# Performance work log

Measured on AMD Instinct MI355X. Metric: run time of the kernel, lower is better.

The kernel has to match this reference:

```python
import jax, jax.numpy as jnp
import numpy as np
from jax import lax

B, L = 2, 1024
D_MODEL, D_STATE, EXPAND, D_CONV = 1024, 16, 2, 4
D_INNER = EXPAND * D_MODEL            # 2048
DT_RANK = (D_MODEL + 15) // 16        # 64


def setup_inputs() -> dict:
    key = jax.random.key(0)
    ks = jax.random.split(key, 8)
    g = lambda k, shape, s=0.02: jax.random.normal(k, shape, dtype=jnp.float32) * s
    # Mamba-style A init: A = -exp(A_log), A_log = log(1..d_state) per channel
    A_log = jnp.log(jnp.broadcast_to(
        jnp.arange(1, D_STATE + 1, dtype=jnp.float32), (D_INNER, D_STATE)))
    return {
        "x": jax.random.normal(ks[0], (B, L, D_MODEL), dtype=jnp.float32),
        "W_in": g(ks[1], (D_MODEL, 2 * D_INNER)),
        "conv_w": g(ks[2], (D_INNER, D_CONV), 0.1),
        "conv_b": jnp.zeros((D_INNER,), jnp.float32),
        "W_x": g(ks[3], (D_INNER, DT_RANK + 2 * D_STATE)),
        "W_dt": g(ks[4], (DT_RANK, D_INNER)),
        "b_dt": g(ks[5], (D_INNER,), 0.1),
        "A_log": A_log,
        "D_skip": jnp.ones((D_INNER,), jnp.float32),
        "W_out": g(ks[6], (D_INNER, D_MODEL)),
    }


def reference(x, W_in, conv_w, conv_b, W_x, W_dt, b_dt, A_log, D_skip, W_out):
    # in_proj -> (u, z): [B, L, D_INNER] each
    xz = x @ W_in
    u, z = xz[..., :D_INNER], xz[..., D_INNER:]

    # causal depthwise conv1d, kernel D_CONV (small fixed loop over taps)
    up = jnp.pad(u, ((0, 0), (D_CONV - 1, 0), (0, 0)))
    u = sum(up[:, k:k + L, :] * conv_w[:, k] for k in range(D_CONV)) + conv_b
    u = jax.nn.silu(u)

    # input-dependent dt, B, C
    x_dbl = u @ W_x                                    # [B, L, dt_rank + 2N]
    dt = x_dbl[..., :DT_RANK]
    Bm = x_dbl[..., DT_RANK:DT_RANK + D_STATE]         # [B, L, N]
    Cm = x_dbl[..., DT_RANK + D_STATE:]                # [B, L, N]
    delta = jax.nn.softplus(dt @ W_dt + b_dt)          # [B, L, D]

    A = -jnp.exp(A_log)                                # [D, N]
    deltaA = jnp.exp(jnp.einsum('bld,dn->bldn', delta, A))   # [B, L, D, N]
    dBu = (delta * u)[..., None] * Bm[:, :, None, :]          # [B, L, D, N]

    def step(h, inp):
        dA_t, dBu_t, c_t = inp                         # [B,D,N],[B,D,N],[B,N]
        h = dA_t * h + dBu_t
        y_t = jnp.einsum('bdn,bn->bd', h, c_t)
        return h, y_t

    h0 = jnp.zeros((B, D_INNER, D_STATE), x.dtype)
    _, ys = lax.scan(step, h0,
                     (deltaA.transpose(1, 0, 2, 3),
                      dBu.transpose(1, 0, 2, 3),
                      Cm.transpose(1, 0, 2)))
    y = ys.transpose(1, 0, 2) + u * D_skip             # [B, L, D_INNER]
    y = y * jax.nn.silu(z)                             # gated output
    return y @ W_out                                   # [B, L, D_MODEL]
```

## Files before the change

kernel.cpp:

```cpp
#include <hip/hip_runtime.h>


typedef unsigned short u16;
typedef unsigned int   u32;

#define B_SZ 2
#define L_SZ 1024
#define DM   1024
#define DI   2048
#define DS   16
#define DTR  64
#define NXD  96
#define NCHUNK 16
#define CL   64
#define KSPLIT 8
#define KC     256
#define OSPLIT 4

typedef __bf16 bf16x8 __attribute__((ext_vector_type(8)));
typedef float  f32x4  __attribute__((ext_vector_type(4)));

__device__ __forceinline__ u16 f2bf(float f) {
    u32 x = __float_as_uint(f);
    x += 0x7fffu + ((x >> 16) & 1u);
    return (u16)(x >> 16);
}
__device__ __forceinline__ float bf2f(u16 v) {
    return __uint_as_float(((u32)v) << 16);
}

__device__ __forceinline__ void gld_lds16(const u16* g, u16* l) {
    __builtin_amdgcn_global_load_lds(
        (const __attribute__((address_space(1))) u32*)g,
        (__attribute__((address_space(3))) u32*)l, 16, 0, 0);
}

__global__ __launch_bounds__(256) void gemm128u2(
    const u16* __restrict__ A, const u16* __restrict__ BT,
    float* __restrict__ Cf, u16* __restrict__ Cb,
    const float* __restrict__ bias,
    int M, int N, int K, int KCHUNK, int op)
{
    __shared__ u16 As0[128 * 32];
    __shared__ u16 Bs0[128 * 32];
    __shared__ u16 As1[128 * 32];
    __shared__ u16 Bs1[128 * 32];

    const int tid  = threadIdx.x;
    const int wave = tid >> 6;
    const int lane = tid & 63;
    const int q    = lane >> 4;
    const int r16  = lane & 15;
    const int wm   = (wave & 1) * 64;
    const int wn   = (wave >> 1) * 64;
    const int m0   = blockIdx.y * 128;
    const int n0   = blockIdx.x * 128;
    const int srow = tid >> 2;
    const int sseg = (tid & 3) * 8;
    const int kb   = blockIdx.z * KCHUNK;

    const u16* gA0 = A  + (size_t)(m0 + srow)      * K + sseg;
    const u16* gA1 = A  + (size_t)(m0 + 64 + srow) * K + sseg;
    const u16* gB0 = BT + (size_t)(n0 + srow)      * K + sseg;
    const u16* gB1 = BT + (size_t)(n0 + 64 + srow) * K + sseg;
    u16* lA0 = As0 + tid * 8;  u16* lA0b = As0 + 2048 + tid * 8;
    u16* lB0 = Bs0 + tid * 8;  u16* lB0b = Bs0 + 2048 + tid * 8;
    u16* lA1 = As1 + tid * 8;  u16* lA1b = As1 + 2048 + tid * 8;
    u16* lB1 = Bs1 + tid * 8;  u16* lB1b = Bs1 + 2048 + tid * 8;

    f32x4 acc[4][4];
#pragma unroll
    for (int s = 0; s < 4; ++s)
#pragma unroll
        for (int j = 0; j < 4; ++j) acc[s][j] = (f32x4){0.f, 0.f, 0.f, 0.f};

    for (int k0 = kb; k0 < kb + KCHUNK; k0 += 64) {
        __syncthreads();
        gld_lds16(gA0 + k0, lA0);
        gld_lds16(gA1 + k0, lA0b);
        gld_lds16(gB0 + k0, lB0);
        gld_lds16(gB1 + k0, lB0b);
        gld_lds16(gA0 + k0 + 32, lA1);
        gld_lds16(gA1 + k0 + 32, lA1b);
        gld_lds16(gB0 + k0 + 32, lB1);
        gld_lds16(gB1 + k0 + 32, lB1b);
        __syncthreads();

        bf16x8 af[4], bfr[4];
#pragma unroll
        for (int s = 0; s < 4; ++s)
            af[s] = *(const bf16x8*)(As0 + (wm + s * 16 + r16) * 32 + q * 8);
#pragma unroll
        for (int j = 0; j < 4; ++j)
            bfr[j] = *(const bf16x8*)(Bs0 + (wn + j * 16 + r16) * 32 + q * 8);
#pragma unroll
        for (int s = 0; s < 4; ++s)
#pragma unroll
            for (int j = 0; j < 4; ++j)
                acc[s][j] = __builtin_amdgcn_mfma_f32_16x16x32_bf16(
                    af[s], bfr[j], acc[s][j], 0, 0, 0);
#pragma unroll
        for (int s = 0; s < 4; ++s)
            af[s] = *(const bf16x8*)(As1 + (wm + s * 16 + r16) * 32 + q * 8);
#pragma unroll
        for (int j = 0; j < 4; ++j)
            bfr[j] = *(const bf16x8*)(Bs1 + (wn + j * 16 + r16) * 32 + q * 8);
#pragma unroll
        for (int s = 0; s < 4; ++s)
#pragma unroll
            for (int j = 0; j < 4; ++j)
                acc[s][j] = __builtin_amdgcn_mfma_f32_16x16x32_bf16(
                    af[s], bfr[j], acc[s][j], 0, 0, 0);
    }

#pragma unroll
    for (int s = 0; s < 4; ++s) {
        const int row0 = m0 + wm + s * 16 + q * 4;
#pragma unroll
        for (int j = 0; j < 4; ++j) {
            const int col = n0 + wn + j * 16 + r16;
            if (op == 0) {
                float* Cz = Cf + (size_t)blockIdx.z * M * N;
#pragma unroll
                for (int i = 0; i < 4; ++i)
                    Cz[(size_t)(row0 + i) * N + col] = acc[s][j][i];
            } else if (op == 1) {
                const float bv = bias[col];
#pragma unroll
                for (int i = 0; i < 4; ++i) {
                    float v = acc[s][j][i] + bv;
                    v = (v > 20.f) ? v : log1pf(__expf(v));
                    Cf[(size_t)(row0 + i) * N + col] = v;
                }
            } else {
#pragma unroll
                for (int i = 0; i < 4; ++i)
                    Cb[(size_t)(row0 + i) * N + col] = f2bf(acc[s][j][i]);
            }
        }
    }
}

__global__ __launch_bounds__(256) void reduce_out(
    const float* __restrict__ part, float* __restrict__ out, int n)
{
    const int i = (blockIdx.x * 256 + threadIdx.x) * 4;
    if (i >= n) return;
    f32x4 v = *(const f32x4*)(part + i);
#pragma unroll
    for (int s = 1; s < OSPLIT; ++s) {
        f32x4 p = *(const f32x4*)(part + (size_t)s * n + i);
        v.x += p.x; v.y += p.y; v.z += p.z; v.w += p.w;
    }
    *(f32x4*)(out + i) = v;
}

__global__ __launch_bounds__(256) void gemm_skinny_splitk(
    const u16* __restrict__ A, const u16* __restrict__ BT,
    float* __restrict__ Cpart, int M, int N, int K)
{
    constexpr int LDT = 40;
    __shared__ u16 As[128 * LDT];
    __shared__ u16 Bs[64 * LDT];

    const int tid  = threadIdx.x;
    const int wave = tid >> 6;
    const int lane = tid & 63;
    const int q    = lane >> 4;
    const int r16  = lane & 15;
    const int m0   = blockIdx.y * 128;
    const int n0   = blockIdx.x * 64;
    const int kcs  = blockIdx.z * KC;
    const int sr   = tid >> 2;
    const int ss   = (tid & 3) * 8;

    f32x4 acc[2][4];
#pragma unroll
    for (int s = 0; s < 2; ++s)
#pragma unroll
        for (int j = 0; j < 4; ++j) acc[s][j] = (f32x4){0.f, 0.f, 0.f, 0.f};

    const int  bcol   = n0 + sr;
    const bool bvalid = bcol < N;

    for (int k0 = kcs; k0 < kcs + KC; k0 += 32) {
        __syncthreads();
        uint4 a0 = *(const uint4*)(A + (size_t)(m0 + sr)      * K + k0 + ss);
        uint4 a1 = *(const uint4*)(A + (size_t)(m0 + 64 + sr) * K + k0 + ss);
        uint4 bv = make_uint4(0u, 0u, 0u, 0u);
        if (bvalid) bv = *(const uint4*)(BT + (size_t)bcol * K + k0 + ss);
        *(uint4*)(As + sr * LDT + ss)        = a0;
        *(uint4*)(As + (64 + sr) * LDT + ss) = a1;
        *(uint4*)(Bs + sr * LDT + ss)        = bv;
        __syncthreads();

        bf16x8 af[2], bfr[4];
#pragma unroll
        for (int s = 0; s < 2; ++s)
            af[s] = *(const bf16x8*)(As + (wave * 32 + s * 16 + r16) * LDT + q * 8);
#pragma unroll
        for (int j = 0; j < 4; ++j)
            bfr[j] = *(const bf16x8*)(Bs + (j * 16 + r16) * LDT + q * 8);
#pragma unroll
        for (int s = 0; s < 2; ++s)
#pragma unroll
            for (int j = 0; j < 4; ++j)
                acc[s][j] = __builtin_amdgcn_mfma_f32_16x16x32_bf16(
                    af[s], bfr[j], acc[s][j], 0, 0, 0);
    }

    float* Cp = Cpart + (size_t)blockIdx.z * M * N;
#pragma unroll
    for (int s = 0; s < 2; ++s) {
        const int row0 = m0 + wave * 32 + s * 16 + q * 4;
#pragma unroll
        for (int j = 0; j < 4; ++j) {
            const int col = n0 + j * 16 + r16;
            if (col < N) {
#pragma unroll
                for (int i = 0; i < 4; ++i)
                    Cp[(size_t)(row0 + i) * N + col] = acc[s][j][i];
            }
        }
    }
}

__global__ __launch_bounds__(256) void reduce_xdbl(
    const float* __restrict__ part, float* __restrict__ xdbl,
    u16* __restrict__ dtbf)
{
    const int i = blockIdx.x * 256 + threadIdx.x;
    const int row = i / NXD, col = i - row * NXD;
    float v = 0.f;
#pragma unroll
    for (int s = 0; s < KSPLIT; ++s)
        v += part[(size_t)s * (B_SZ * L_SZ * NXD) + i];
    xdbl[i] = v;
    if (col < DTR) dtbf[row * DTR + col] = f2bf(v);
}

__device__ __forceinline__ void tr_tile(
    const float* __restrict__ in, u16* __restrict__ out,
    int R, int C, int tr, int tc, int tid, float (*t)[33])
{
    const int tx = tid & 31, ty = tid >> 5;
    const int r0 = tr * 32, c0 = tc * 32;
#pragma unroll
    for (int i = 0; i < 4; ++i) {
        int r = r0 + ty + i * 8, c = c0 + tx;
        if (r < R && c < C) t[ty + i * 8][tx] = in[(size_t)r * C + c];
    }
    __syncthreads();
#pragma unroll
    for (int i = 0; i < 4; ++i) {
        int oR = c0 + ty + i * 8, oC = r0 + tx;
        if (oR < C && oC < R) out[(size_t)oR * R + oC] = f2bf(t[tx][ty + i * 8]);
    }
}

__global__ __launch_bounds__(256) void prep_kernel(
    const float* __restrict__ x,     u16* __restrict__ xbf,
    const float* __restrict__ W_in,  u16* __restrict__ winT,
    const float* __restrict__ W_out, u16* __restrict__ woutT,
    const float* __restrict__ W_x,   u16* __restrict__ wxT,
    const float* __restrict__ W_dt,  u16* __restrict__ wdtT)
{
    __shared__ float t[32][33];
    const int id  = blockIdx.x;
    const int tid = threadIdx.x;
    if (id < 4096) {
        tr_tile(W_in, winT, 1024, 4096, id >> 7, id & 127, tid, t);
    } else if (id < 6144) {
        int i2 = id - 4096;
        tr_tile(W_out, woutT, 2048, 1024, i2 >> 5, i2 & 31, tid, t);
    } else if (id < 6336) {
        int i3 = id - 6144;
        tr_tile(W_x, wxT, 2048, 96, i3 / 3, i3 % 3, tid, t);
    } else if (id < 6464) {
        int i4 = id - 6336;
        tr_tile(W_dt, wdtT, 64, 2048, i4 >> 6, i4 & 63, tid, t);
    } else {
        int i = (id - 6464) * 256 + tid;
        xbf[i] = f2bf(x[i]);
    }
}

__global__ __launch_bounds__(256) void conv_silu_kernel(
    const u16* __restrict__ xzbf, const float* __restrict__ cw,
    const float* __restrict__ cb, u16* __restrict__ ucbf)
{
    const int idx = blockIdx.x * 256 + threadIdx.x;
    const int d   = idx & (DI - 1);
    const int pos = idx >> 11;
    const int l   = pos & (L_SZ - 1);
    float s = cb[d];
#pragma unroll
    for (int k = 0; k < 4; ++k) {
        int ls = l + k - 3;
        if (ls >= 0)
            s = fmaf(bf2f(xzbf[(size_t)(pos + k - 3) * (2 * DI) + d]), cw[d * 4 + k], s);
    }
    float v = s / (1.f + __expf(-s));
    ucbf[idx] = f2bf(v);
}

__global__ __launch_bounds__(256) void scan_pass1(
    const float* __restrict__ delta, const u16* __restrict__ ucbf,
    const float* __restrict__ xdbl, const float* __restrict__ A_log,
    float* __restrict__ hbuf, float* __restrict__ pbuf)
{
    const int c = blockIdx.x;
    const int d = blockIdx.y * 256 + threadIdx.x;
    const int b = blockIdx.z;
    float Av[16], h[16], P[16];
#pragma unroll
    for (int n = 0; n < 16; ++n) {
        Av[n] = -__expf(A_log[d * 16 + n]);
        h[n] = 0.f; P[n] = 1.f;
    }
    const int rowbase = b * L_SZ + c * CL;
    for (int i = 0; i < CL; ++i) {
        const int row = rowbase + i;
        float dlt = delta[(size_t)row * DI + d];
        float uu  = bf2f(ucbf[(size_t)row * DI + d]);
        float du  = dlt * uu;
        const float* xr = xdbl + (size_t)row * NXD;
#pragma unroll
        for (int n = 0; n < 16; ++n) {
            float e = __expf(dlt * Av[n]);
            P[n] *= e;
            h[n] = fmaf(e, h[n], du * xr[DTR + n]);
        }
    }
    size_t base = ((size_t)((b * NCHUNK + c) * DI + d)) * 16;
#pragma unroll
    for (int n = 0; n < 16; ++n) { hbuf[base + n] = h[n]; pbuf[base + n] = P[n]; }
}

__global__ __launch_bounds__(256) void scan_pass2(
    float* __restrict__ hbuf, const float* __restrict__ pbuf)
{
    const int j = blockIdx.x * 256 + threadIdx.x;
    const int b = blockIdx.y;
    float h0 = 0.f;
    for (int cc = 0; cc < NCHUNK; ++cc) {
        size_t o = ((size_t)(b * NCHUNK + cc)) * (DI * 16) + j;
        float hl = hbuf[o];
        float Pl = pbuf[o];
        hbuf[o] = h0;
        h0 = fmaf(Pl, h0, hl);
    }
}

__global__ __launch_bounds__(256) void scan_pass3(
    const float* __restrict__ delta, const u16* __restrict__ ucbf,
    const float* __restrict__ xdbl, const float* __restrict__ A_log,
    const float* __restrict__ hbuf, const u16* __restrict__ xzbf,
    const float* __restrict__ Dskip, u16* __restrict__ ybf)
{
    const int c = blockIdx.x;
    const int d = blockIdx.y * 256 + threadIdx.x;
    const int b = blockIdx.z;
    float Av[16], h[16];
    size_t base = ((size_t)((b * NCHUNK + c) * DI + d)) * 16;
#pragma unroll
    for (int n = 0; n < 16; ++n) {
        Av[n] = -__expf(A_log[d * 16 + n]);
        h[n]  = hbuf[base + n];
    }
    const float Dk = Dskip[d];
    const int rowbase = b * L_SZ + c * CL;
    for (int i = 0; i < CL; ++i) {
        const int row = rowbase + i;
        float dlt = delta[(size_t)row * DI + d];
        float uu  = bf2f(ucbf[(size_t)row * DI + d]);
        float du  = dlt * uu;
        const float* xr = xdbl + (size_t)row * NXD;
        float y = 0.f;
#pragma unroll
        for (int n = 0; n < 16; ++n) {
            float e = __expf(dlt * Av[n]);
            h[n] = fmaf(e, h[n], du * xr[DTR + n]);
            y = fmaf(h[n], xr[DTR + DS + n], y);
        }
        float zz = bf2f(xzbf[(size_t)row * (2 * DI) + DI + d]);
        float yv = fmaf(uu, Dk, y) * (zz / (1.f + __expf(-zz)));
        ybf[(size_t)row * DI + d] = f2bf(yv);
    }
}

constexpr size_t OFF_DELTA   = 0;
constexpr size_t OFF_XDBL    = OFF_DELTA + 4194304;
constexpr size_t OFF_SCRATCH = OFF_XDBL  + 196608;
constexpr size_t OFF_F32_END = OFF_SCRATCH + 8388608;
constexpr size_t SOFF_XBF   = 0;
constexpr size_t SOFF_WINT  = SOFF_XBF   + 2097152;
constexpr size_t SOFF_XZBF  = SOFF_WINT  + 4194304;
constexpr size_t SOFF_UCBF  = SOFF_XZBF  + 8388608;
constexpr size_t SOFF_WXT   = SOFF_UCBF  + 4194304;
constexpr size_t SOFF_DTBF  = SOFF_WXT   + 196608;
constexpr size_t SOFF_WDTT  = SOFF_DTBF  + 131072;
constexpr size_t SOFF_WOUTT = SOFF_WDTT  + 131072;
constexpr size_t SOFF_YBF   = SOFF_WOUTT + 2097152;

extern "C" void kernel_launch(void* const* d_in, const int* in_sizes, int n_in,
                              void* d_out, int out_size, void* d_ws, size_t ws_size,
                              hipStream_t stream)
{
    const float* x     = (const float*)d_in[0];
    const float* W_in  = (const float*)d_in[1];
    const float* cw    = (const float*)d_in[2];
    const float* cb    = (const float*)d_in[3];
    const float* W_x   = (const float*)d_in[4];
    const float* W_dt  = (const float*)d_in[5];
    const float* b_dt  = (const float*)d_in[6];
    const float* A_log = (const float*)d_in[7];
    const float* Dsk   = (const float*)d_in[8];
    const float* W_out = (const float*)d_in[9];
    float* out = (float*)d_out;

    float* wsf   = (float*)d_ws;
    float* dlt   = wsf + OFF_DELTA;
    float* xdbl  = wsf + OFF_XDBL;
    float* xpart = wsf + OFF_SCRATCH;
    float* hbuf  = wsf + OFF_SCRATCH;
    float* pbuf  = wsf + OFF_SCRATCH + 1048576;
    float* opart = wsf + OFF_SCRATCH;
    u16* sb    = (u16*)(wsf + OFF_F32_END);
    u16* xbf   = sb + SOFF_XBF;
    u16* winT  = sb + SOFF_WINT;
    u16* xzbf  = sb + SOFF_XZBF;
    u16* ucbf  = sb + SOFF_UCBF;
    u16* wxT   = sb + SOFF_WXT;
    u16* dtbf  = sb + SOFF_DTBF;
    u16* wdtT  = sb + SOFF_WDTT;
    u16* woutT = sb + SOFF_WOUTT;
    u16* ybf   = sb + SOFF_YBF;

    prep_kernel<<<14656, 256, 0, stream>>>(x, xbf, W_in, winT, W_out, woutT,
                                           W_x, wxT, W_dt, wdtT);

    gemm128u2<<<dim3(32, 16, 1), 256, 0, stream>>>(
        xbf, winT, nullptr, xzbf, nullptr, 2048, 4096, 1024, 1024, 2);

    conv_silu_kernel<<<(B_SZ * L_SZ * DI) / 256, 256, 0, stream>>>(xzbf, cw, cb, ucbf);

    gemm_skinny_splitk<<<dim3(2, 16, KSPLIT), 256, 0, stream>>>(
        ucbf, wxT, xpart, 2048, NXD, 2048);
    reduce_xdbl<<<(B_SZ * L_SZ * NXD) / 256, 256, 0, stream>>>(xpart, xdbl, dtbf);

    gemm128u2<<<dim3(16, 16, 1), 256, 0, stream>>>(
        dtbf, wdtT, dlt, nullptr, b_dt, 2048, 2048, 64, 64, 1);

    scan_pass1<<<dim3(NCHUNK, DI / 256, B_SZ), 256, 0, stream>>>(dlt, ucbf, xdbl, A_log, hbuf, pbuf);
    scan_pass2<<<dim3(DI * 16 / 256, B_SZ), 256, 0, stream>>>(hbuf, pbuf);
    scan_pass3<<<dim3(NCHUNK, DI / 256, B_SZ), 256, 0, stream>>>(dlt, ucbf, xdbl, A_log, hbuf, xzbf, Dsk, ybf);

    gemm128u2<<<dim3(8, 16, OSPLIT), 256, 0, stream>>>(
        ybf, woutT, opart, nullptr, nullptr, 2048, 1024, 2048, 2048 / OSPLIT, 0);
    reduce_out<<<(2048 * 1024 / 4 + 255) / 256, 256, 0, stream>>>(
        opart, out, 2048 * 1024);
}
```

Measured before the change: 280.8 us.

## Software-pipeline GEMM loads with 4-stage LDS ring and register prefetch

Replaces the double-buffered 128x128 GEMM, which fully drained and synced around every load, with a 4-stage LDS ring buffer. It issues async global-to-LDS loads three tiles ahead and uses explicit vmcnt waits plus raw barriers. The skinny split-K GEMM now prefetches the next tile into registers while the current one is in LDS, clamping the out-of-range B column instead of branching. The out-projection split-K drops from 4 to 2, which halves the partial buffers to reduce, but leaves fewer blocks. The hand-coded waitcnt encodings and barrier placement are fragile and tied to the gfx target.

```diff
diff --git a/kernel.cpp b/kernel.cpp
--- a/kernel.cpp
+++ b/kernel.cpp
@@ -15,7 +15,7 @@
 #define CL   64
 #define KSPLIT 8
 #define KC     256
-#define OSPLIT 4
+#define OSPLIT 2
 
 typedef __bf16 bf16x8 __attribute__((ext_vector_type(8)));
 typedef float  f32x4  __attribute__((ext_vector_type(4)));
@@ -35,16 +35,25 @@
         (__attribute__((address_space(3))) u32*)l, 16, 0, 0);
 }
 
-__global__ __launch_bounds__(256) void gemm128u2(
+__device__ __forceinline__ void wg_barrier() {
+    __asm__ volatile("" ::: "memory");
+    __builtin_amdgcn_s_barrier();
+    __asm__ volatile("" ::: "memory");
+}
+#define WAIT_VM12() __builtin_amdgcn_s_waitcnt(0xF7C)
+#define WAIT_VM8()  __builtin_amdgcn_s_waitcnt(0xF78)
+#define WAIT_VM4()  __builtin_amdgcn_s_waitcnt(0xF74)
+#define WAIT_VM0()  __builtin_amdgcn_s_waitcnt(0xF70)
+#define WAIT_LGKM0() __builtin_amdgcn_s_waitcnt(0xC07F)
+
+__global__ __launch_bounds__(256) void gemm128p(
     const u16* __restrict__ A, const u16* __restrict__ BT,
     float* __restrict__ Cf, u16* __restrict__ Cb,
     const float* __restrict__ bias,
     int M, int N, int K, int KCHUNK, int op)
 {
-    __shared__ u16 As0[128 * 32];
-    __shared__ u16 Bs0[128 * 32];
-    __shared__ u16 As1[128 * 32];
-    __shared__ u16 Bs1[128 * 32];
+    __shared__ u16 As[4][128 * 32];
+    __shared__ u16 Bs[4][128 * 32];
 
     const int tid  = threadIdx.x;
     const int wave = tid >> 6;
@@ -55,18 +64,23 @@
     const int wn   = (wave >> 1) * 64;
     const int m0   = blockIdx.y * 128;
     const int n0   = blockIdx.x * 128;
-    const int srow = tid >> 2;
-    const int sseg = (tid & 3) * 8;
     const int kb   = blockIdx.z * KCHUNK;
 
-    const u16* gA0 = A  + (size_t)(m0 + srow)      * K + sseg;
-    const u16* gA1 = A  + (size_t)(m0 + 64 + srow) * K + sseg;
-    const u16* gB0 = BT + (size_t)(n0 + srow)      * K + sseg;
-    const u16* gB1 = BT + (size_t)(n0 + 64 + srow) * K + sseg;
-    u16* lA0 = As0 + tid * 8;  u16* lA0b = As0 + 2048 + tid * 8;
-    u16* lB0 = Bs0 + tid * 8;  u16* lB0b = Bs0 + 2048 + tid * 8;
-    u16* lA1 = As1 + tid * 8;  u16* lA1b = As1 + 2048 + tid * 8;
-    u16* lB1 = Bs1 + tid * 8;  u16* lB1b = Bs1 + 2048 + tid * 8;
+    const u16* gA0 = A  + (size_t)(m0 + (tid >> 2))      * K + (tid & 3) * 8;
+    const u16* gA1 = A  + (size_t)(m0 + 64 + (tid >> 2)) * K + (tid & 3) * 8;
+    const u16* gB0 = BT + (size_t)(n0 + (tid >> 2))      * K + (tid & 3) * 8;
+    const u16* gB1 = BT + (size_t)(n0 + 64 + (tid >> 2)) * K + (tid & 3) * 8;
+
+    const int niter = KCHUNK >> 5;
+
+    const int pre = niter < 3 ? niter : 3;
+    for (int p = 0; p < pre; ++p) {
+        const int k0 = kb + p * 32;
+        gld_lds16(gA0 + k0, &As[p][tid * 8]);
+        gld_lds16(gA1 + k0, &As[p][2048 + tid * 8]);
+        gld_lds16(gB0 + k0, &Bs[p][tid * 8]);
+        gld_lds16(gB1 + k0, &Bs[p][2048 + tid * 8]);
+    }
 
     f32x4 acc[4][4];
 #pragma unroll
@@ -74,43 +88,40 @@
 #pragma unroll
         for (int j = 0; j < 4; ++j) acc[s][j] = (f32x4){0.f, 0.f, 0.f, 0.f};
 
-    for (int k0 = kb; k0 < kb + KCHUNK; k0 += 64) {
-        __syncthreads();
-        gld_lds16(gA0 + k0, lA0);
-        gld_lds16(gA1 + k0, lA0b);
-        gld_lds16(gB0 + k0, lB0);
-        gld_lds16(gB1 + k0, lB0b);
-        gld_lds16(gA0 + k0 + 32, lA1);
-        gld_lds16(gA1 + k0 + 32, lA1b);
-        gld_lds16(gB0 + k0 + 32, lB1);
-        gld_lds16(gB1 + k0 + 32, lB1b);
-        __syncthreads();
-
+    for (int it = 0; it < niter; ++it) {
+        if (it + 3 < niter) {
+            const int k0 = kb + (it + 3) * 32;
+            const int bi = (it + 3) & 3;
+            gld_lds16(gA0 + k0, &As[bi][tid * 8]);
+            gld_lds16(gA1 + k0, &As[bi][2048 + tid * 8]);
+            gld_lds16(gB0 + k0, &Bs[bi][tid * 8]);
+            gld_lds16(gB1 + k0, &Bs[bi][2048 + tid * 8]);
+            WAIT_VM12();
+        } else if (it + 2 < niter) {
+            WAIT_VM8();
+        } else if (it + 1 < niter) {
+            WAIT_VM4();
+        } else {
+            WAIT_VM0();
+        }
+        wg_barrier();
+
+        const int cur = it & 3;
         bf16x8 af[4], bfr[4];
 #pragma unroll
         for (int s = 0; s < 4; ++s)
-            af[s] = *(const bf16x8*)(As0 + (wm + s * 16 + r16) * 32 + q * 8);
+            af[s] = *(const bf16x8*)(&As[cur][(wm + s * 16 + r16) * 32 + q * 8]);
 #pragma unroll
         for (int j = 0; j < 4; ++j)
-            bfr[j] = *(const bf16x8*)(Bs0 + (wn + j * 16 + r16) * 32 + q * 8);
+            bfr[j] = *(const bf16x8*)(&Bs[cur][(wn + j * 16 + r16) * 32 + q * 8]);
 #pragma unroll
         for (int s = 0; s < 4; ++s)
 #pragma unroll
             for (int j = 0; j < 4; ++j)
                 acc[s][j] = __builtin_amdgcn_mfma_f32_16x16x32_bf16(
                     af[s], bfr[j], acc[s][j], 0, 0, 0);
-#pragma unroll
-        for (int s = 0; s < 4; ++s)
-            af[s] = *(const bf16x8*)(As1 + (wm + s * 16 + r16) * 32 + q * 8);
-#pragma unroll
-        for (int j = 0; j < 4; ++j)
-            bfr[j] = *(const bf16x8*)(Bs1 + (wn + j * 16 + r16) * 32 + q * 8);
-#pragma unroll
-        for (int s = 0; s < 4; ++s)
-#pragma unroll
-            for (int j = 0; j < 4; ++j)
-                acc[s][j] = __builtin_amdgcn_mfma_f32_16x16x32_bf16(
-                    af[s], bfr[j], acc[s][j], 0, 0, 0);
+
+        wg_barrier();
     }
 
 #pragma unroll
@@ -180,19 +191,25 @@
 #pragma unroll
         for (int j = 0; j < 4; ++j) acc[s][j] = (f32x4){0.f, 0.f, 0.f, 0.f};
 
-    const int  bcol   = n0 + sr;
-    const bool bvalid = bcol < N;
-
-    for (int k0 = kcs; k0 < kcs + KC; k0 += 32) {
-        __syncthreads();
-        uint4 a0 = *(const uint4*)(A + (size_t)(m0 + sr)      * K + k0 + ss);
-        uint4 a1 = *(const uint4*)(A + (size_t)(m0 + 64 + sr) * K + k0 + ss);
-        uint4 bv = make_uint4(0u, 0u, 0u, 0u);
-        if (bvalid) bv = *(const uint4*)(BT + (size_t)bcol * K + k0 + ss);
+    const int bcol  = n0 + sr;
+    const int bcolc = bcol < N ? bcol : N - 1;
+
+    constexpr int NIT = KC / 32;
+    uint4 a0 = *(const uint4*)(A + (size_t)(m0 + sr)      * K + kcs + ss);
+    uint4 a1 = *(const uint4*)(A + (size_t)(m0 + 64 + sr) * K + kcs + ss);
+    uint4 bv = *(const uint4*)(BT + (size_t)bcolc * K + kcs + ss);
+
+    for (int it = 0; it < NIT; ++it) {
+        wg_barrier();
         *(uint4*)(As + sr * LDT + ss)        = a0;
         *(uint4*)(As + (64 + sr) * LDT + ss) = a1;
         *(uint4*)(Bs + sr * LDT + ss)        = bv;
-        __syncthreads();
+        const int kn = (it + 1 < NIT) ? (kcs + (it + 1) * 32) : kcs;
+        a0 = *(const uint4*)(A + (size_t)(m0 + sr)      * K + kn + ss);
+        a1 = *(const uint4*)(A + (size_t)(m0 + 64 + sr) * K + kn + ss);
+        bv = *(const uint4*)(BT + (size_t)bcolc * K + kn + ss);
+        WAIT_LGKM0();
+        wg_barrier();
 
         bf16x8 af[2], bfr[4];
 #pragma unroll
@@ -440,7 +457,7 @@
     prep_kernel<<<14656, 256, 0, stream>>>(x, xbf, W_in, winT, W_out, woutT,
                                            W_x, wxT, W_dt, wdtT);
 
-    gemm128u2<<<dim3(32, 16, 1), 256, 0, stream>>>(
+    gemm128p<<<dim3(32, 16, 1), 256, 0, stream>>>(
         xbf, winT, nullptr, xzbf, nullptr, 2048, 4096, 1024, 1024, 2);
 
     conv_silu_kernel<<<(B_SZ * L_SZ * DI) / 256, 256, 0, stream>>>(xzbf, cw, cb, ucbf);
@@ -449,14 +466,14 @@
         ucbf, wxT, xpart, 2048, NXD, 2048);
     reduce_xdbl<<<(B_SZ * L_SZ * NXD) / 256, 256, 0, stream>>>(xpart, xdbl, dtbf);
 
-    gemm128u2<<<dim3(16, 16, 1), 256, 0, stream>>>(
+    gemm128p<<<dim3(16, 16, 1), 256, 0, stream>>>(
         dtbf, wdtT, dlt, nullptr, b_dt, 2048, 2048, 64, 64, 1);
 
     scan_pass1<<<dim3(NCHUNK, DI / 256, B_SZ), 256, 0, stream>>>(dlt, ucbf, xdbl, A_log, hbuf, pbuf);
     scan_pass2<<<dim3(DI * 16 / 256, B_SZ), 256, 0, stream>>>(hbuf, pbuf);
     scan_pass3<<<dim3(NCHUNK, DI / 256, B_SZ), 256, 0, stream>>>(dlt, ucbf, xdbl, A_log, hbuf, xzbf, Dsk, ybf);
 
-    gemm128u2<<<dim3(8, 16, OSPLIT), 256, 0, stream>>>(
+    gemm128p<<<dim3(8, 16, OSPLIT), 256, 0, stream>>>(
         ybf, woutT, opart, nullptr, nullptr, 2048, 1024, 2048, 2048 / OSPLIT, 0);
     reduce_out<<<(2048 * 1024 / 4 + 255) / 256, 256, 0, stream>>>(
         opart, out, 2048 * 1024);
```

Result: no change. 284.2 us (+1.2%).
